# Optimization experiments

Hardware: AMD Instinct MI355X
Metric: run time of the kernel (lower is better)

Reference implementation:

```python
import jax, jax.numpy as jnp
import numpy as np

EMB = 1024
NH = 16
DH = EMB // NH
SCALE = np.sqrt(EMB).astype(np.float32)  # module scales by sqrt(emb_dim), not sqrt(d_head)


def setup_inputs() -> dict:
    key = jax.random.key(0)
    ks = jax.random.split(key, 9)
    s = 1.0 / np.sqrt(EMB)
    return {
        "a": jax.random.normal(ks[0], (4, 2048, EMB), jnp.float32),
        "Wq": jax.random.normal(ks[1], (EMB, EMB), jnp.float32) * s,
        "bq": jnp.zeros((EMB,), jnp.float32),
        "Wk": jax.random.normal(ks[2], (EMB, EMB), jnp.float32) * s,
        "bk": jnp.zeros((EMB,), jnp.float32),
        "Wv": jax.random.normal(ks[3], (EMB, EMB), jnp.float32) * s,
        "bv": jnp.zeros((EMB,), jnp.float32),
        "Wo": jax.random.normal(ks[4], (EMB, EMB), jnp.float32) * s,
        "bo": jnp.zeros((EMB,), jnp.float32),
    }


def reference(a, Wq, bq, Wk, bk, Wv, bv, Wo, bo):
    N, S, _ = a.shape
    # Q/K/V projections (self-attention: b is None -> b = a)
    Q = (a @ Wq + bq).reshape(N, S, NH, DH).transpose(0, 2, 1, 3)  # [N,H,A,D]
    K = (a @ Wk + bk).reshape(N, S, NH, DH).transpose(0, 2, 1, 3)  # [N,H,B,D]
    V = (a @ Wv + bv).reshape(N, S, NH, DH).transpose(0, 2, 1, 3)  # [N,H,B,D]
    score = jnp.einsum('nhad,nhbd->nhab', Q, K) / SCALE
    score = jax.nn.softmax(score, axis=-1)
    out = jnp.einsum('nhab,nhbd->nhad', score, V)                  # [N,H,A,D]
    out = out.transpose(0, 2, 1, 3).reshape(N, S, EMB)
    return out @ Wo + bo
```

## Files before the change

kernel.cpp:

```cpp
#include <hip/hip_runtime.h>
#include <hip/hip_bf16.h>
#include <stdint.h>

typedef __attribute__((ext_vector_type(8))) short short8v;
typedef __attribute__((ext_vector_type(4))) float float4v;

#define GLDS16(gp, lp) __builtin_amdgcn_global_load_lds( \
    (const __attribute__((address_space(1))) void*)(gp),  \
    (__attribute__((address_space(3))) void*)(lp), 16, 0, 0)

#if __has_builtin(__builtin_amdgcn_exp2f)
#define EXP2(x) __builtin_amdgcn_exp2f(x)
#else
#define EXP2(x) exp2f(x)
#endif

#define LOG2E 1.4426950408889634f

__global__ __launch_bounds__(256) void cast_a_kernel(
    const float* __restrict__ src, __hip_bfloat16* __restrict__ dst, int n4) {
  int i = blockIdx.x * blockDim.x + threadIdx.x;
  if (i < n4) {
    float4 v = ((const float4*)src)[i];
    union { __hip_bfloat16 h[4]; ushort4 u; } p;
    p.h[0] = __float2bfloat16(v.x);
    p.h[1] = __float2bfloat16(v.y);
    p.h[2] = __float2bfloat16(v.z);
    p.h[3] = __float2bfloat16(v.w);
    ((ushort4*)dst)[i] = p.u;
  }
}

__global__ __launch_bounds__(256) void transpose4_kernel(
    const float* __restrict__ Wq, const float* __restrict__ Wk,
    const float* __restrict__ Wv, const float* __restrict__ Wo,
    __hip_bfloat16* __restrict__ Wcat, __hip_bfloat16* __restrict__ WoT) {
  __shared__ float t[32][33];
  const int z = blockIdx.z;
  const float* W = (z == 0) ? Wq : (z == 1) ? Wk : (z == 2) ? Wv : Wo;
  __hip_bfloat16* dst = (z < 3) ? (Wcat + (size_t)z * 1048576) : WoT;
  int tx = threadIdx.x & 31, ty = threadIdx.x >> 5;
  int r0 = blockIdx.y * 32, c0 = blockIdx.x * 32;
#pragma unroll
  for (int i = 0; i < 4; ++i) {
    int r = ty + i * 8;
    t[r][tx] = W[(size_t)(r0 + r) * 1024 + c0 + tx];
  }
  __syncthreads();
#pragma unroll
  for (int i = 0; i < 4; ++i) {
    int r = ty + i * 8;
    dst[(size_t)(c0 + r) * 1024 + r0 + tx] = __float2bfloat16(t[tx][r]);
  }
}

__global__ __launch_bounds__(512, 2) void gemm_qkv8_kernel(
    const __hip_bfloat16* __restrict__ A, const __hip_bfloat16* __restrict__ BT,
    const float* __restrict__ bq, const float* __restrict__ bk,
    const float* __restrict__ bv, __hip_bfloat16* __restrict__ Qh,
    __hip_bfloat16* __restrict__ Kh, __hip_bfloat16* __restrict__ Vt) {
  __shared__ char lds[131072];
  const int tid = threadIdx.x;
  const int l = tid & 63, w = tid >> 6;
  const int g = l >> 4, cc = l & 15;
  const int wm = w >> 2, wn = w & 3;
  const int sw = (cc & 7) << 4;
  const int bid = blockIdx.x;
  const int nbid = (bid & 7) * 48 + (bid >> 3);
  const int tm = nbid / 12, tn = nbid % 12;
  const int m0 = tm * 256, n0 = tn * 256;

  const int scol = ((tid & 7) * 16) ^ (((tid >> 3) & 7) << 4);
  const char* pA = (const char*)A + (size_t)(m0 + (tid >> 3)) * 2048 + scol;
  const char* pB = (const char*)BT + (size_t)(n0 + (tid >> 3)) * 2048 + scol;
  char* ldsT = lds + tid * 16;

#define STGH(pG, base, half, kt) {                                            \
    GLDS16((pG) + ((half) * 128) * 2048 + (kt) * 128,                         \
           ldsT + (base) + (half) * 16384);                                   \
    GLDS16((pG) + ((half) * 128 + 64) * 2048 + (kt) * 128,                    \
           ldsT + (base) + (half) * 16384 + 8192);                            \
  }

  short8v af[4][2], bf[4][2];
#define DSA(base, fmb)                                                        \
  _Pragma("unroll") for (int i = 0; i < 4; ++i)                               \
  _Pragma("unroll") for (int kk = 0; kk < 2; ++kk)                            \
    af[i][kk] = *(const short8v*)(lds + (base) +                              \
        (((wm * 128 + ((fmb) + i) * 16 + cc) * 128 + kk * 64 + g * 16) ^ sw));
#define DSB(base, np)                                                         \
  _Pragma("unroll") for (int ii = 0; ii < 2; ++ii)                            \
  _Pragma("unroll") for (int kk = 0; kk < 2; ++kk)                            \
    bf[(np) * 2 + ii][kk] = *(const short8v*)(lds + (base) +                  \
        (((wn * 64 + ((np) * 2 + ii) * 16 + cc) * 128 + kk * 64 + g * 16) ^ sw));

  float4v acc[8][4];
#pragma unroll
  for (int m = 0; m < 8; ++m)
#pragma unroll
    for (int n = 0; n < 4; ++n) acc[m][n] = (float4v){0.f, 0.f, 0.f, 0.f};

#define MM(fmb, np)                                                           \
  __builtin_amdgcn_s_setprio(1);                                              \
  _Pragma("unroll") for (int i = 0; i < 4; ++i)                               \
  _Pragma("unroll") for (int ii = 0; ii < 2; ++ii)                            \
  _Pragma("unroll") for (int kk = 0; kk < 2; ++kk)                            \
    acc[(fmb) + i][(np) * 2 + ii] = __builtin_amdgcn_mfma_f32_16x16x32_bf16(  \
        af[i][kk], bf[(np) * 2 + ii][kk], acc[(fmb) + i][(np) * 2 + ii], 0, 0, 0); \
  __builtin_amdgcn_s_setprio(0);

#define BAR() __builtin_amdgcn_s_barrier()
#define WAIT4() asm volatile("s_waitcnt vmcnt(4)" ::: "memory")

  STGH(pB, 65536, 0, 0); STGH(pB, 65536, 1, 0);
  STGH(pA, 0, 0, 0);     STGH(pA, 0, 1, 0);
  STGH(pB, 98304, 0, 1); STGH(pB, 98304, 1, 1);
  WAIT4();
  BAR();

  for (int j = 0; j < 8; ++j) {
    const int vv = 2 * j + 1;
    const int u2 = (j < 7) ? 2 * j + 2 : 15;
    const int v2 = (j < 7) ? 2 * j + 3 : 15;
    DSA(0, 0); DSB(65536, 0);
    STGH(pA, 32768, 0, vv);
    BAR(); MM(0, 0); BAR();
    DSB(65536, 1);
    STGH(pA, 32768, 1, vv);
    BAR(); MM(0, 1); BAR();
    DSA(0, 4);
    STGH(pB, 65536, 0, u2);
    BAR(); MM(4, 0); BAR();
    STGH(pB, 65536, 1, u2);
    WAIT4();
    BAR(); MM(4, 1); BAR();
    DSA(32768, 0); DSB(98304, 0);
    STGH(pA, 0, 0, u2);
    BAR(); MM(0, 0); BAR();
    DSB(98304, 1);
    STGH(pA, 0, 1, u2);
    BAR(); MM(0, 1); BAR();
    DSA(32768, 4);
    STGH(pB, 98304, 0, v2);
    BAR(); MM(4, 0); BAR();
    STGH(pB, 98304, 1, v2);
    WAIT4();
    BAR(); MM(4, 1); BAR();
  }
#undef STGH
#undef DSA
#undef DSB
#undef MM
#undef BAR
#undef WAIT4

  const int sec = n0 >> 10;
  if (sec < 2) {
    __hip_bfloat16* out = sec == 0 ? Qh : Kh;
    const float* bias = sec == 0 ? bq : bk;
    const float scale = sec == 0 ? (LOG2E / 32.f) : 1.f;
#pragma unroll
    for (int m = 0; m < 8; ++m) {
#pragma unroll
      for (int n = 0; n < 4; ++n) {
        int colc = (n0 + wn * 64 + n * 16 + cc) & 1023;
        float b = bias[colc];
        int h = colc >> 6, d = colc & 63;
#pragma unroll
        for (int r = 0; r < 4; ++r) {
          int grow = m0 + wm * 128 + m * 16 + g * 4 + r;
          int nb = grow >> 11, s = grow & 2047;
          out[((size_t)(nb * 16 + h) * 2048 + s) * 64 + d] =
              __float2bfloat16((acc[m][n][r] + b) * scale);
        }
      }
    }
  } else {
#pragma unroll
    for (int m = 0; m < 8; ++m) {
      int grow0 = m0 + wm * 128 + m * 16 + g * 4;
      int nb = grow0 >> 11, key0 = grow0 & 2047;
      int kp0 = (key0 & ~31) | ((key0 & 12) << 1) | (((key0 >> 4) & 1) << 2);
#pragma unroll
      for (int n = 0; n < 4; ++n) {
        int colc = (n0 + wn * 64 + n * 16 + cc) & 1023;
        float b = bv[colc];
        int h = colc >> 6, d = colc & 63;
        union { __hip_bfloat16 h4[4]; uint2 u; } pk;
#pragma unroll
        for (int r = 0; r < 4; ++r) pk.h4[r] = __float2bfloat16(acc[m][n][r] + b);
        *(uint2*)&Vt[((size_t)((nb * 16 + h) * 64 + d)) * 2048 + kp0] = pk.u;
      }
    }
  }
}

__global__ __launch_bounds__(256, 2) void gemm_o_kernel(
    const __hip_bfloat16* __restrict__ A, const __hip_bfloat16* __restrict__ BT,
    const float* __restrict__ bias, float* __restrict__ C) {
  __shared__ char lds[32768];
  const int tid = threadIdx.x;
  const int l = tid & 63, w = tid >> 6;
  const int g = l >> 4, cc = l & 15;
  const int bid = blockIdx.x;
  const int nbid = (bid & 7) * 64 + (bid >> 3);
  const int m0 = (nbid & 63) * 128, n0 = (nbid >> 6) * 128;
  const int wm = w >> 1, wn = w & 1;

  float4v acc[4][4];
#pragma unroll
  for (int m = 0; m < 4; ++m)
#pragma unroll
    for (int n = 0; n < 4; ++n) acc[m][n] = (float4v){0.f, 0.f, 0.f, 0.f};

  for (int kt = 0; kt < 16; ++kt) {
#pragma unroll
    for (int j = 0; j < 4; ++j) {
      int ci = (w * 4 + j) * 64 + l;
      int row = ci >> 3, ko = (ci & 7) * 16;
      GLDS16((const char*)A + (size_t)(m0 + row) * 2048 + kt * 128 + ko,
             lds + ci * 16);
      GLDS16((const char*)BT + (size_t)(n0 + row) * 2048 + kt * 128 + ko,
             lds + 16384 + ci * 16);
    }
    __syncthreads();
#pragma unroll
    for (int h = 0; h < 2; ++h) {
      short8v af[4], bf[4];
#pragma unroll
      for (int m = 0; m < 4; ++m)
        af[m] = *(const short8v*)(lds + (wm * 64 + m * 16 + cc) * 128 + h * 64 + g * 16);
#pragma unroll
      for (int n = 0; n < 4; ++n)
        bf[n] = *(const short8v*)(lds + 16384 + (wn * 64 + n * 16 + cc) * 128 + h * 64 + g * 16);
#pragma unroll
      for (int m = 0; m < 4; ++m)
#pragma unroll
        for (int n = 0; n < 4; ++n)
          acc[m][n] = __builtin_amdgcn_mfma_f32_16x16x32_bf16(af[m], bf[n], acc[m][n], 0, 0, 0);
    }
    __syncthreads();
  }

#pragma unroll
  for (int m = 0; m < 4; ++m) {
    int row = m0 + wm * 64 + m * 16 + g * 4;
#pragma unroll
    for (int n = 0; n < 4; ++n) {
      int col = n0 + wn * 64 + n * 16 + cc;
      float b = bias[col];
#pragma unroll
      for (int r = 0; r < 4; ++r)
        C[(size_t)(row + r) * 1024 + col] = acc[m][n][r] + b;
    }
  }
}

__global__ __launch_bounds__(512, 4) void attn_kernel(
    const __hip_bfloat16* __restrict__ Q,
    const __hip_bfloat16* __restrict__ K,
    const __hip_bfloat16* __restrict__ VT,
    __hip_bfloat16* __restrict__ AO) {
  __shared__ char sK[3][8192];
  __shared__ char sV[3][8192];
  const int tid = threadIdx.x;
  const int l = tid & 63, w = tid >> 6;
  const int g = l >> 4, cc = l & 15;
  const int bid = blockIdx.x;
  const int nbid = (bid & 7) * 64 + (bid >> 3);
  const int bx = nbid & 7, nh = nbid >> 3;
  const int q0 = bx * 256 + w * 32;
  const char* Kb = (const char*)(K + (size_t)nh * 131072);
  const char* Vb = (const char*)(VT + (size_t)nh * 131072);
  const __hip_bfloat16* Qb = Q + (size_t)nh * 131072;

  short8v qf[2][2];
#pragma unroll
  for (int qg = 0; qg < 2; ++qg)
#pragma unroll
    for (int dh = 0; dh < 2; ++dh)
      qf[qg][dh] = *(const short8v*)(Qb + (size_t)(q0 + qg * 16 + cc) * 64 + dh * 32 + g * 8);

  int koff[4][2], voff[4][2];
#pragma unroll
  for (int kg = 0; kg < 4; ++kg)
#pragma unroll
    for (int dh = 0; dh < 2; ++dh) {
      int row = kg * 16 + cc;
      koff[kg][dh] = (row * 128 + dh * 64 + g * 16) ^ ((row & 7) << 4);
    }
#pragma unroll
  for (int f = 0; f < 4; ++f)
#pragma unroll
    for (int hh = 0; hh < 2; ++hh) {
      int d = f * 16 + cc;
      voff[f][hh] = (d * 128 + hh * 64 + g * 16) ^ ((d & 7) << 4);
    }
  const int ss = tid * 16;
  const int sr = ss >> 7;
  const int soff = (ss & 127) ^ ((sr & 7) << 4);
  const int stKo = sr * 128 + soff;
  const int stVo = sr * 4096 + soff;

  const short8v fone = {16256, 16256, 16256, 16256, 16256, 16256, 16256, 16256};

  float lr[2] = {0.f, 0.f};
  float4v oacc[2][4];
#pragma unroll
  for (int qg = 0; qg < 2; ++qg)
#pragma unroll
    for (int f = 0; f < 4; ++f) oacc[qg][f] = (float4v){0.f, 0.f, 0.f, 0.f};

#define STAGE(kb, vb, ktv)                                                    \
  {                                                                           \
    GLDS16(Kb + (size_t)(ktv) * 8192 + stKo, (kb) + ss);                      \
    GLDS16(Vb + (size_t)(ktv) * 128 + stVo, (vb) + ss);                       \
  }

  char *k0 = sK[0], *k1 = sK[1], *k2 = sK[2];
  char *v0 = sV[0], *v1 = sV[1], *v2 = sV[2];
  STAGE(k0, v0, 0);
  STAGE(k1, v1, 1);

  for (int kt = 0; kt < 32; ++kt) {
    if (kt < 31) {
      asm volatile("s_waitcnt vmcnt(2)" ::: "memory");
    } else {
      asm volatile("s_waitcnt vmcnt(0)" ::: "memory");
    }
    __builtin_amdgcn_s_barrier();
    if (kt < 30) STAGE(k2, v2, kt + 2);
    const char* sKc = k0;
    const char* sVc = v0;

    short8v kf[4][2];
#pragma unroll
    for (int kg = 0; kg < 4; ++kg)
#pragma unroll
      for (int dh = 0; dh < 2; ++dh)
        kf[kg][dh] = *(const short8v*)(sKc + koff[kg][dh]);

    short8v pf[2][2];
#pragma unroll
    for (int qg = 0; qg < 2; ++qg) {
      float4v sv[4];
#pragma unroll
      for (int kg = 0; kg < 4; ++kg) {
        float4v z = (float4v){0.f, 0.f, 0.f, 0.f};
        z = __builtin_amdgcn_mfma_f32_16x16x32_bf16(kf[kg][0], qf[qg][0], z, 0, 0, 0);
        sv[kg] = __builtin_amdgcn_mfma_f32_16x16x32_bf16(kf[kg][1], qf[qg][1], z, 0, 0, 0);
      }
#pragma unroll
      for (int kg = 0; kg < 4; ++kg)
#pragma unroll
        for (int r = 0; r < 4; ++r) sv[kg][r] = EXP2(sv[kg][r]);
#pragma unroll
      for (int hh = 0; hh < 2; ++hh) {
        union { __hip_bfloat16 h[8]; short8v v8; } pk;
#pragma unroll
        for (int j = 0; j < 4; ++j) {
          pk.h[j]     = __float2bfloat16(sv[2 * hh][j]);
          pk.h[4 + j] = __float2bfloat16(sv[2 * hh + 1][j]);
        }
        pf[qg][hh] = pk.v8;
      }
      float4v t = (float4v){0.f, 0.f, 0.f, 0.f};
      t = __builtin_amdgcn_mfma_f32_16x16x32_bf16(fone, pf[qg][0], t, 0, 0, 0);
      t = __builtin_amdgcn_mfma_f32_16x16x32_bf16(fone, pf[qg][1], t, 0, 0, 0);
      lr[qg] += t[0];
    }

#pragma unroll
    for (int f = 0; f < 4; ++f)
#pragma unroll
      for (int hh = 0; hh < 2; ++hh) {
        short8v vk = *(const short8v*)(sVc + voff[f][hh]);
#pragma unroll
        for (int qg = 0; qg < 2; ++qg)
          oacc[qg][f] = __builtin_amdgcn_mfma_f32_16x16x32_bf16(vk, pf[qg][hh], oacc[qg][f], 0, 0, 0);
      }

    char* tt;
    tt = k0; k0 = k1; k1 = k2; k2 = tt;
    tt = v0; v0 = v1; v1 = v2; v2 = tt;
  }
#undef STAGE

  int nb = nh >> 4, h = nh & 15;
#pragma unroll
  for (int qg = 0; qg < 2; ++qg) {
    float inv = 1.f / lr[qg];
    int qrow = q0 + qg * 16 + cc;
#pragma unroll
    for (int f = 0; f < 4; ++f)
#pragma unroll
      for (int r = 0; r < 4; ++r) {
        int d = f * 16 + g * 4 + r;
        AO[(size_t)(nb * 2048 + qrow) * 1024 + h * 64 + d] =
            __float2bfloat16(oacc[qg][f][r] * inv);
      }
  }
}

extern "C" void kernel_launch(void* const* d_in, const int* in_sizes, int n_in,
                              void* d_out, int out_size, void* d_ws, size_t ws_size,
                              hipStream_t stream) {
  const float* a  = (const float*)d_in[0];
  const float* Wq = (const float*)d_in[1];
  const float* bq = (const float*)d_in[2];
  const float* Wk = (const float*)d_in[3];
  const float* bk = (const float*)d_in[4];
  const float* Wv = (const float*)d_in[5];
  const float* bv = (const float*)d_in[6];
  const float* Wo = (const float*)d_in[7];
  const float* bo = (const float*)d_in[8];

  char* ws = (char*)d_ws;
  __hip_bfloat16* aB   = (__hip_bfloat16*)(ws);
  __hip_bfloat16* Wcat = (__hip_bfloat16*)(ws + (16ull << 20));
  __hip_bfloat16* WoT  = (__hip_bfloat16*)(ws + (22ull << 20));
  __hip_bfloat16* Qh   = (__hip_bfloat16*)(ws + (24ull << 20));
  __hip_bfloat16* Kh   = (__hip_bfloat16*)(ws + (40ull << 20));
  __hip_bfloat16* Vt   = (__hip_bfloat16*)(ws + (56ull << 20));
  __hip_bfloat16* AOb  = (__hip_bfloat16*)(ws + (72ull << 20));

  cast_a_kernel<<<8192, 256, 0, stream>>>(a, aB, 8192 * 1024 / 4);
  dim3 tg(32, 32, 4);
  transpose4_kernel<<<tg, 256, 0, stream>>>(Wq, Wk, Wv, Wo, Wcat, WoT);

  gemm_qkv8_kernel<<<384, 512, 0, stream>>>(aB, Wcat, bq, bk, bv, Qh, Kh, Vt);

  attn_kernel<<<512, 512, 0, stream>>>(Qh, Kh, Vt, AOb);

  gemm_o_kernel<<<512, 256, 0, stream>>>(AOb, WoT, bo, (float*)d_out);
}
```

Measured before the change: 178.6 us.

## Software-pipeline attention loop: overlap QK^T of next tile with PV of previous

Restructures the attention inner loop so each iteration computes QK^T for tile t, then PV for tile t-1 using the previous tile's probabilities, then exp/pack for tile t. A prologue handles the first QK and an epilogue the last PV. V gets a fourth LDS buffer so the previous tile's V stays resident. The intent is to hide the exp and convert latency behind independent MFMA work, at the cost of more registers and more LDS per block, which may reduce occupancy.

```diff
diff --git a/kernel.cpp b/kernel.cpp
--- a/kernel.cpp
+++ b/kernel.cpp
@@ -88,7 +88,7 @@
   _Pragma("unroll") for (int kk = 0; kk < 2; ++kk)                            \
     af[i][kk] = *(const short8v*)(lds + (base) +                              \
         (((wm * 128 + ((fmb) + i) * 16 + cc) * 128 + kk * 64 + g * 16) ^ sw));
-#define DSB(base, np)                                                         \
+#define DSB(base, np)                                                        \
   _Pragma("unroll") for (int ii = 0; ii < 2; ++ii)                            \
   _Pragma("unroll") for (int kk = 0; kk < 2; ++kk)                            \
     bf[(np) * 2 + ii][kk] = *(const short8v*)(lds + (base) +                  \
@@ -262,7 +262,7 @@
     const __hip_bfloat16* __restrict__ VT,
     __hip_bfloat16* __restrict__ AO) {
   __shared__ char sK[3][8192];
-  __shared__ char sV[3][8192];
+  __shared__ char sV[4][8192];
   const int tid = threadIdx.x;
   const int l = tid & 63, w = tid >> 6;
   const int g = l >> 4, cc = l & 15;
@@ -317,74 +317,93 @@
     GLDS16(Vb + (size_t)(ktv) * 128 + stVo, (vb) + ss);                       \
   }
 
-  char *k0 = sK[0], *k1 = sK[1], *k2 = sK[2];
-  char *v0 = sV[0], *v1 = sV[1], *v2 = sV[2];
-  STAGE(k0, v0, 0);
-  STAGE(k1, v1, 1);
-
-  for (int kt = 0; kt < 32; ++kt) {
-    if (kt < 31) {
+#define QKBLK(KSRC, SV)                                                       \
+  {                                                                           \
+    short8v kf_[4][2];                                                        \
+    _Pragma("unroll") for (int kg = 0; kg < 4; ++kg)                          \
+    _Pragma("unroll") for (int dh = 0; dh < 2; ++dh)                          \
+      kf_[kg][dh] = *(const short8v*)((KSRC) + koff[kg][dh]);                 \
+    _Pragma("unroll") for (int qg = 0; qg < 2; ++qg)                          \
+    _Pragma("unroll") for (int kg = 0; kg < 4; ++kg) {                        \
+      float4v z_ = (float4v){0.f, 0.f, 0.f, 0.f};                             \
+      z_ = __builtin_amdgcn_mfma_f32_16x16x32_bf16(kf_[kg][0], qf[qg][0], z_, 0, 0, 0); \
+      (SV)[qg][kg] = __builtin_amdgcn_mfma_f32_16x16x32_bf16(kf_[kg][1], qf[qg][1], z_, 0, 0, 0); \
+    }                                                                         \
+  }
+
+#define PVBLK(VSRC)                                                           \
+  {                                                                           \
+    _Pragma("unroll") for (int f = 0; f < 4; ++f)                             \
+    _Pragma("unroll") for (int hh = 0; hh < 2; ++hh) {                        \
+      short8v vk_ = *(const short8v*)((VSRC) + voff[f][hh]);                  \
+      _Pragma("unroll") for (int qg = 0; qg < 2; ++qg)                        \
+        oacc[qg][f] = __builtin_amdgcn_mfma_f32_16x16x32_bf16(vk_, pfP[qg][hh], oacc[qg][f], 0, 0, 0); \
+    }                                                                         \
+    _Pragma("unroll") for (int qg = 0; qg < 2; ++qg) {                        \
+      float4v t_ = (float4v){0.f, 0.f, 0.f, 0.f};                             \
+      t_ = __builtin_amdgcn_mfma_f32_16x16x32_bf16(fone, pfP[qg][0], t_, 0, 0, 0); \
+      t_ = __builtin_amdgcn_mfma_f32_16x16x32_bf16(fone, pfP[qg][1], t_, 0, 0, 0); \
+      lr[qg] += t_[0];                                                        \
+    }                                                                         \
+  }
+
+#define SMBLK(SV)                                                             \
+  {                                                                           \
+    _Pragma("unroll") for (int qg = 0; qg < 2; ++qg) {                        \
+      _Pragma("unroll") for (int kg = 0; kg < 4; ++kg)                        \
+      _Pragma("unroll") for (int r = 0; r < 4; ++r)                           \
+        (SV)[qg][kg][r] = EXP2((SV)[qg][kg][r]);                              \
+      _Pragma("unroll") for (int hh = 0; hh < 2; ++hh) {                      \
+        union { __hip_bfloat16 h[8]; short8v v8; } pk_;                       \
+        _Pragma("unroll") for (int j = 0; j < 4; ++j) {                       \
+          pk_.h[j]     = __float2bfloat16((SV)[qg][2 * hh][j]);               \
+          pk_.h[4 + j] = __float2bfloat16((SV)[qg][2 * hh + 1][j]);           \
+        }                                                                     \
+        pfP[qg][hh] = pk_.v8;                                                 \
+      }                                                                       \
+    }                                                                         \
+  }
+
+  short8v pfP[2][2];
+  char *kc = sK[0], *kn = sK[1], *ks = sK[2];
+  char *vp = sV[0], *vc = sV[1], *vn = sV[2], *vs = sV[3];
+
+  STAGE(sK[0], sV[0], 0);
+  STAGE(sK[1], sV[1], 1);
+  asm volatile("s_waitcnt vmcnt(2)" ::: "memory");
+  __builtin_amdgcn_s_barrier();
+  STAGE(sK[2], sV[2], 2);
+  {
+    float4v sv[2][4];
+    QKBLK(sK[0], sv);
+    SMBLK(sv);
+  }
+  kc = sK[1]; kn = sK[2]; ks = sK[0];
+  vp = sV[0]; vc = sV[1]; vn = sV[2]; vs = sV[3];
+
+  for (int t = 1; t <= 31; ++t) {
+    if (t < 31) {
       asm volatile("s_waitcnt vmcnt(2)" ::: "memory");
     } else {
       asm volatile("s_waitcnt vmcnt(0)" ::: "memory");
     }
     __builtin_amdgcn_s_barrier();
-    if (kt < 30) STAGE(k2, v2, kt + 2);
-    const char* sKc = k0;
-    const char* sVc = v0;
-
-    short8v kf[4][2];
-#pragma unroll
-    for (int kg = 0; kg < 4; ++kg)
-#pragma unroll
-      for (int dh = 0; dh < 2; ++dh)
-        kf[kg][dh] = *(const short8v*)(sKc + koff[kg][dh]);
-
-    short8v pf[2][2];
-#pragma unroll
-    for (int qg = 0; qg < 2; ++qg) {
-      float4v sv[4];
-#pragma unroll
-      for (int kg = 0; kg < 4; ++kg) {
-        float4v z = (float4v){0.f, 0.f, 0.f, 0.f};
-        z = __builtin_amdgcn_mfma_f32_16x16x32_bf16(kf[kg][0], qf[qg][0], z, 0, 0, 0);
-        sv[kg] = __builtin_amdgcn_mfma_f32_16x16x32_bf16(kf[kg][1], qf[qg][1], z, 0, 0, 0);
-      }
-#pragma unroll
-      for (int kg = 0; kg < 4; ++kg)
-#pragma unroll
-        for (int r = 0; r < 4; ++r) sv[kg][r] = EXP2(sv[kg][r]);
-#pragma unroll
-      for (int hh = 0; hh < 2; ++hh) {
-        union { __hip_bfloat16 h[8]; short8v v8; } pk;
-#pragma unroll
-        for (int j = 0; j < 4; ++j) {
-          pk.h[j]     = __float2bfloat16(sv[2 * hh][j]);
-          pk.h[4 + j] = __float2bfloat16(sv[2 * hh + 1][j]);
-        }
-        pf[qg][hh] = pk.v8;
-      }
-      float4v t = (float4v){0.f, 0.f, 0.f, 0.f};
-      t = __builtin_amdgcn_mfma_f32_16x16x32_bf16(fone, pf[qg][0], t, 0, 0, 0);
-      t = __builtin_amdgcn_mfma_f32_16x16x32_bf16(fone, pf[qg][1], t, 0, 0, 0);
-      lr[qg] += t[0];
-    }
-
-#pragma unroll
-    for (int f = 0; f < 4; ++f)
-#pragma unroll
-      for (int hh = 0; hh < 2; ++hh) {
-        short8v vk = *(const short8v*)(sVc + voff[f][hh]);
-#pragma unroll
-        for (int qg = 0; qg < 2; ++qg)
-          oacc[qg][f] = __builtin_amdgcn_mfma_f32_16x16x32_bf16(vk, pf[qg][hh], oacc[qg][f], 0, 0, 0);
-      }
+    if (t <= 29) STAGE(ks, vs, t + 2);
+
+    float4v sv[2][4];
+    QKBLK(kc, sv);
+    PVBLK(vp);
+    SMBLK(sv);
 
     char* tt;
-    tt = k0; k0 = k1; k1 = k2; k2 = tt;
-    tt = v0; v0 = v1; v1 = v2; v2 = tt;
-  }
+    tt = kc; kc = kn; kn = ks; ks = tt;
+    tt = vp; vp = vc; vc = vn; vn = vs; vs = tt;
+  }
+  PVBLK(vp);
 #undef STAGE
+#undef QKBLK
+#undef PVBLK
+#undef SMBLK
 
   int nb = nh >> 4, h = nh & 15;
 #pragma unroll
```

After: 184.9 us. 1.04x slower.
